# Kernel tuning notes

Measured on AMD Instinct MI355X. Metric: run time of the kernel, lower is better.

Reference implementation:

```python
import jax, jax.numpy as jnp
import numpy as np

B, H0, W0, C = 8, 112, 112, 192
NH, WS, SS = 6, 7, 3
HID = 4 * C


def _rel_pos_index(ws):
    coords = np.stack(np.meshgrid(np.arange(ws), np.arange(ws), indexing='ij'))  # [2,ws,ws]
    flat = coords.reshape(2, -1)
    rel = flat[:, :, None] - flat[:, None, :]          # [2,N,N]
    rel = rel.transpose(1, 2, 0).copy()                # [N,N,2]
    rel[:, :, 0] += ws - 1
    rel[:, :, 1] += ws - 1
    rel[:, :, 0] *= 2 * ws - 1
    return rel.sum(-1)                                 # [N,N]


def _attn_mask(Hp, Wp, ws, ss):
    # 0 / -100 mask for shifted windows, identical to torch get_attn_mask
    img = np.zeros((Hp, Wp))
    cnt = 0
    for hs in (slice(0, -ws), slice(-ws, -ss), slice(-ss, None)):
        for wsl in (slice(0, -ws), slice(-ws, -ss), slice(-ss, None)):
            img[hs, wsl] = cnt
            cnt += 1
    mw = img.reshape(Hp // ws, ws, Wp // ws, ws).transpose(0, 2, 1, 3).reshape(-1, ws * ws)
    am = mw[:, None, :] - mw[:, :, None]
    return np.where(am != 0, np.float32(-100.0), np.float32(0.0)).astype(np.float32)  # [nW,N,N]


def _ln(x, g, b, eps=1e-5):
    mu = jnp.mean(x, axis=-1, keepdims=True)
    var = jnp.mean(jnp.square(x - mu), axis=-1, keepdims=True)
    return (x - mu) * jax.lax.rsqrt(var + eps) * g + b


def setup_inputs() -> dict:
    key = jax.random.key(0)
    ks = jax.random.split(key, 8)
    p = lambda k, s: jax.random.normal(k, s, jnp.float32) * 0.02
    return {
        'query': jax.random.normal(ks[0], (B, H0 * W0, C), jnp.float32),
        'norm1_g': jnp.ones((C,), jnp.float32), 'norm1_b': jnp.zeros((C,), jnp.float32),
        'qkv_w': p(ks[1], (C, 3 * C)), 'qkv_b': jnp.zeros((3 * C,), jnp.float32),
        'rpb_table': p(ks[2], ((2 * WS - 1) ** 2, NH)),
        'proj_w': p(ks[3], (C, C)), 'proj_b': jnp.zeros((C,), jnp.float32),
        'norm2_g': jnp.ones((C,), jnp.float32), 'norm2_b': jnp.zeros((C,), jnp.float32),
        'fc1_w': p(ks[4], (C, HID)), 'fc1_b': jnp.zeros((HID,), jnp.float32),
        'fc2_w': p(ks[5], (HID, C)), 'fc2_b': jnp.zeros((C,), jnp.float32),
        'H': H0, 'W': W0,
    }


def reference(query, norm1_g, norm1_b, qkv_w, qkv_b, rpb_table, proj_w, proj_b,
              norm2_g, norm2_b, fc1_w, fc1_b, fc2_w, fc2_b, H, W):
    Bq, L, Cq = query.shape
    ws, ss, nh = WS, SS, NH
    hd = Cq // nh
    N = ws * ws
    # ---- W-MSA branch ----
    x = _ln(query, norm1_g, norm1_b).reshape(Bq, H, W, Cq)
    # H, W chosen divisible by ws -> pad branch is a no-op
    x = jnp.roll(x, (-ss, -ss), axis=(1, 2))            # cyclic shift
    nWh, nWw = H // ws, W // ws
    # window partition -> [B*nW, N, C]
    xw = x.reshape(Bq, nWh, ws, nWw, ws, Cq).transpose(0, 1, 3, 2, 4, 5).reshape(-1, N, Cq)
    qkv = (xw @ qkv_w + qkv_b).reshape(-1, N, 3, nh, hd).transpose(2, 0, 3, 1, 4)
    q, k, v = qkv[0] * (hd ** -0.5), qkv[1], qkv[2]     # [B_,nh,N,hd]
    attn = jnp.einsum('bhnd,bhmd->bhnm', q, k)
    bias = rpb_table[_rel_pos_index(ws).reshape(-1)].reshape(N, N, nh).transpose(2, 0, 1)
    attn = attn + bias[None]
    mask = jnp.asarray(_attn_mask(H, W, ws, ss))        # [nW,N,N]
    nW = mask.shape[0]
    attn = attn.reshape(Bq, nW, nh, N, N) + mask[None, :, None]
    attn = jax.nn.softmax(attn.reshape(-1, nh, N, N), axis=-1)
    out = jnp.einsum('bhnm,bhmd->bhnd', attn, v).transpose(0, 2, 1, 3).reshape(-1, N, Cq)
    out = out @ proj_w + proj_b
    # window reverse + reverse shift
    x = out.reshape(Bq, nWh, nWw, ws, ws, Cq).transpose(0, 1, 3, 2, 4, 5).reshape(Bq, H, W, Cq)
    x = jnp.roll(x, (ss, ss), axis=(1, 2)).reshape(Bq, H * W, Cq)
    x = query + x
    # ---- MLP branch ----
    h = _ln(x, norm2_g, norm2_b)
    h = jax.nn.gelu(h @ fc1_w + fc1_b, approximate=False)
    return x + (h @ fc2_w + fc2_b)
```

## Files before the change

kernel.cpp:

```cpp
#include <hip/hip_runtime.h>
#include <hip/hip_bf16.h>
#include <math.h>

using bf16 = __hip_bfloat16;
typedef __bf16 bf16x8 __attribute__((ext_vector_type(8)));
typedef __bf16 bf16x4 __attribute__((ext_vector_type(4)));
typedef float floatx4 __attribute__((ext_vector_type(4)));

__device__ __forceinline__ float bf2f(bf16 x) { return __bfloat162float(x); }
__device__ __forceinline__ bf16 f2bf(float x) { return __float2bfloat16(x); }

__device__ __forceinline__ float loadExt(const void* p, long i, int f32) {
  return f32 ? ((const float*)p)[i] : bf2f(((const bf16*)p)[i]);
}
__device__ __forceinline__ void storeExt(void* p, long i, int f32, float v) {
  if (f32) ((float*)p)[i] = v;
  else     ((bf16*)p)[i] = f2bf(v);
}

#define GLOAD16(gp, lp)                                                       \
  __builtin_amdgcn_global_load_lds(                                           \
      (const __attribute__((address_space(1))) void*)(gp),                    \
      (__attribute__((address_space(3))) void*)(lp), 16, 0, 0)

__global__ void detect_kernel(const unsigned int* __restrict__ q, int* __restrict__ flag) {
  const int lane = threadIdx.x;
  const unsigned int w = q[lane];
  const unsigned int lo = w & 0xffffu;
  const unsigned int e = (lo >> 7) & 0xffu;
  const bool ok = (lo == 0u) || (e >= 100u && e <= 141u);
  const unsigned long long m = __ballot(ok);
  if (lane == 0) flag[0] = (__popcll(m) == 64) ? 1 : 0;
}

__global__ void cvt_params_kernel(const int* __restrict__ flagp,
                                  const void* qkv_b, const void* proj_b,
                                  const void* n1g, const void* n1b,
                                  const void* n2g, const void* n2b,
                                  const void* fc1_b, const void* fc2_b,
                                  const void* rpb, bf16* __restrict__ dst) {
  const int f32 = (flagp[0] == 0);
  int i = blockIdx.x * blockDim.x + threadIdx.x;
  if (i >= 3510) return;
  const void* src; int j = i;
  if      (j < 576)  { src = qkv_b; }
  else if ((j -= 576)  < 192) { src = proj_b; }
  else if ((j -= 192)  < 192) { src = n1g; }
  else if ((j -= 192)  < 192) { src = n1b; }
  else if ((j -= 192)  < 192) { src = n2g; }
  else if ((j -= 192)  < 192) { src = n2b; }
  else if ((j -= 192)  < 768) { src = fc1_b; }
  else if ((j -= 768)  < 192) { src = fc2_b; }
  else { j -= 192; src = rpb; }
  dst[i] = f2bf(loadExt(src, j, f32));
}

__global__ void cvtT_kernel(const int* __restrict__ flagp, const void* __restrict__ src,
                            bf16* __restrict__ dst, int K, int N) {
  const int f32 = (flagp[0] == 0);
  int i = blockIdx.x * blockDim.x + threadIdx.x;
  if (i >= K * N) return;
  int n = i / K, k = i - n * K;
  dst[i] = f2bf(loadExt(src, (long)k * N + n, f32));
}

__global__ void biastab_kernel(const bf16* __restrict__ rpb,
                               bf16* __restrict__ btab) {
  int i = blockIdx.x * blockDim.x + threadIdx.x;
  if (i >= 6 * 2450) return;
  int head = i / 2450, r = i - head * 2450;
  int n = r / 50, m = r - n * 50;
  float v = 0.f;
  if (n < 49 && m < 49) {
    int r1 = n / 7, c1 = n - 7 * r1, r2 = m / 7, c2 = m - 7 * r2;
    v = bf2f(rpb[((r1 - r2 + 6) * 13 + (c1 - c2 + 6)) * 6 + head]);
  }
  btab[i] = f2bf(v);
}

__global__ __launch_bounds__(256) void ln_kernel(const int* __restrict__ flagp, int ext,
                                                 const void* __restrict__ x,
                                                 const bf16* __restrict__ g,
                                                 const bf16* __restrict__ b,
                                                 bf16* __restrict__ out) {
  const int f32 = ext && (flagp[0] == 0);
  const long row = (long)blockIdx.x * 4 + (threadIdx.x >> 6);
  const int lane = threadIdx.x & 63;
  const long gbase = row * 192;
  float v0 = loadExt(x, gbase + lane, f32);
  float v1 = loadExt(x, gbase + lane + 64, f32);
  float v2 = loadExt(x, gbase + lane + 128, f32);
  float s = v0 + v1 + v2;
  #pragma unroll
  for (int off = 32; off > 0; off >>= 1) s += __shfl_xor(s, off, 64);
  const float mu = s * (1.0f / 192.0f);
  float d0 = v0 - mu, d1 = v1 - mu, d2 = v2 - mu;
  float vv = d0 * d0 + d1 * d1 + d2 * d2;
  #pragma unroll
  for (int off = 32; off > 0; off >>= 1) vv += __shfl_xor(vv, off, 64);
  const float rstd = rsqrtf(vv * (1.0f / 192.0f) + 1e-5f);
  bf16* orow = out + row * 192;
  orow[lane]       = f2bf(d0 * rstd * bf2f(g[lane])       + bf2f(b[lane]));
  orow[lane + 64]  = f2bf(d1 * rstd * bf2f(g[lane + 64])  + bf2f(b[lane + 64]));
  orow[lane + 128] = f2bf(d2 * rstd * bf2f(g[lane + 128]) + bf2f(b[lane + 128]));
}

template <int EPI>
__global__ __launch_bounds__(256) void gemm_bt(const bf16* __restrict__ A,
                                               const bf16* __restrict__ BT,
                                               const bf16* __restrict__ bias,
                                               const int* __restrict__ flagp,
                                               const void* res, int res_ext,
                                               void* out, int out_ext,
                                               int M, int N, int K) {
  __shared__ __align__(16) bf16 As[2][128 * 32];
  __shared__ __align__(16) bf16 Bs[2][64 * 32];
  const int xf32 = (flagp[0] == 0);
  const int tid = threadIdx.x;
  const int wave = tid >> 6;
  const int lane = tid & 63;
  const int l16 = lane & 15;
  const int quad = lane >> 4;

  const int nbn = N >> 6;
  const int cpx = gridDim.x >> 3;
  const int wg = (gridDim.x & 7) ? (int)blockIdx.x
                                 : (blockIdx.x & 7) * cpx + (blockIdx.x >> 3);
  const int mb = wg / nbn;
  const int nb = wg - mb * nbn;
  const long m0 = (long)mb * 128;
  const int n0 = nb << 6;

  const int rS = tid >> 2;
  const int sS = tid & 3;
  const int ss = sS ^ ((rS >> 1) & 3);
  const bf16* gA0 = A + (m0 + rS) * (long)K + ss * 8;
  const bf16* gA1 = A + (m0 + rS + 64) * (long)K + ss * 8;
  const bf16* gB  = BT + (long)(n0 + rS) * K + ss * 8;

  floatx4 acc[2][4];
  #pragma unroll
  for (int i = 0; i < 2; i++)
    #pragma unroll
    for (int j = 0; j < 4; j++) acc[i][j] = (floatx4){0.f, 0.f, 0.f, 0.f};

  const int swz = (quad ^ ((l16 >> 1) & 3)) << 3;
  const int arow = wave * 32 + l16;

  GLOAD16(gA0, &As[0][tid * 8]);
  GLOAD16(gA1, &As[0][(tid + 256) * 8]);
  GLOAD16(gB,  &Bs[0][tid * 8]);
  __syncthreads();

  int cur = 0;
  for (int k0 = 0; k0 < K; k0 += 32) {
    if (k0 + 32 < K) {
      const int nxt = cur ^ 1;
      GLOAD16(gA0 + k0 + 32, &As[nxt][tid * 8]);
      GLOAD16(gA1 + k0 + 32, &As[nxt][(tid + 256) * 8]);
      GLOAD16(gB  + k0 + 32, &Bs[nxt][tid * 8]);
    }
    bf16x8 af[2], bfr[4];
    #pragma unroll
    for (int ms = 0; ms < 2; ms++)
      af[ms] = *(const bf16x8*)&As[cur][(arow + ms * 16) * 32 + swz];
    #pragma unroll
    for (int ns = 0; ns < 4; ns++)
      bfr[ns] = *(const bf16x8*)&Bs[cur][(ns * 16 + l16) * 32 + swz];
    #pragma unroll
    for (int ms = 0; ms < 2; ms++)
      #pragma unroll
      for (int ns = 0; ns < 4; ns++)
        acc[ms][ns] = __builtin_amdgcn_mfma_f32_16x16x32_bf16(bfr[ns], af[ms], acc[ms][ns], 0, 0, 0);
    __syncthreads();
    cur ^= 1;
  }

  #pragma unroll
  for (int ms = 0; ms < 2; ms++) {
    const long row = m0 + wave * 32 + ms * 16 + l16;
    #pragma unroll
    for (int ns = 0; ns < 4; ns++) {
      const int col = n0 + ns * 16 + quad * 4;
      const long idx = row * (long)N + col;
      float v[4];
      #pragma unroll
      for (int r = 0; r < 4; r++) v[r] = acc[ms][ns][r] + bf2f(bias[col + r]);
      if (EPI == 1) {
        #pragma unroll
        for (int r = 0; r < 4; r++)
          v[r] = 0.5f * v[r] * (1.0f + erff(v[r] * 0.70710678118654752f));
      }
      if (EPI == 2) {
        if (res_ext && xf32) {
          const float4 t = *(const float4*)((const float*)res + idx);
          v[0] += t.x; v[1] += t.y; v[2] += t.z; v[3] += t.w;
        } else {
          const bf16x4 t = *(const bf16x4*)((const bf16*)res + idx);
          #pragma unroll
          for (int r = 0; r < 4; r++) v[r] += (float)t[r];
        }
      }
      if (out_ext && xf32) {
        float4 t; t.x = v[0]; t.y = v[1]; t.z = v[2]; t.w = v[3];
        *(float4*)((float*)out + idx) = t;
      } else {
        bf16x4 t;
        #pragma unroll
        for (int r = 0; r < 4; r++) t[r] = (__bf16)v[r];
        *(bf16x4*)((bf16*)out + idx) = t;
      }
    }
  }
}

__global__ __launch_bounds__(64, 3) void attn_kernel(const bf16* __restrict__ qkv,
                                                     const bf16* __restrict__ btab,
                                                     bf16* __restrict__ out) {
  __shared__ __align__(16) __bf16 vshT[32 * 64];
  __shared__ __align__(16) __bf16 psh[64 * 64];
  __shared__ int rowIdx[64];
  __shared__ int regn[64];
  const int lane = threadIdx.x;
  const int q = lane >> 4, l16 = lane & 15;
  const int unit = blockIdx.x;
  const int head = unit % 6;
  const int wIdx = unit / 6;
  const int b = wIdx >> 8;
  const int w2 = wIdx & 255;
  const int wh = w2 >> 4;
  const int ww = w2 & 15;

  {
    const int l = lane < 49 ? lane : 48;
    const int r = l / 7, c = l - 7 * r;
    const int hr = wh * 7 + r;
    const int wr = ww * 7 + c;
    int h = hr + 3; if (h >= 112) h -= 112;
    int w = wr + 3; if (w >= 112) w -= 112;
    rowIdx[lane] = b * 12544 + h * 112 + w;
    const int rh = hr < 105 ? 0 : (hr < 109 ? 1 : 2);
    const int rw = wr < 105 ? 0 : (wr < 109 ? 1 : 2);
    regn[lane] = (lane < 49) ? rh * 3 + rw : 99;
  }
  __syncthreads();

  int ridx[4];
  #pragma unroll
  for (int t = 0; t < 4; t++) ridx[t] = rowIdx[t * 16 + l16];

  #pragma unroll
  for (int ii = 0; ii < 4; ii++) {
    const int i = lane + ii * 64;
    const int j = i >> 2, c = (i & 3) * 8;
    const bf16x8 vv = *(const bf16x8*)&qkv[(long)rowIdx[j] * 576 + 384 + head * 32 + c];
    #pragma unroll
    for (int jj = 0; jj < 8; jj++) {
      const int d = c + jj;
      vshT[d * 64 + (((j >> 3) ^ (d & 7)) << 3) + (j & 7)] = vv[jj];
    }
  }

  floatx4 s[4][4];
  #pragma unroll
  for (int it = 0; it < 4; it++)
    #pragma unroll
    for (int jt = 0; jt < 4; jt++) s[it][jt] = (floatx4){0.f, 0.f, 0.f, 0.f};
  {
    bf16x8 afq[4], bfk[4];
    #pragma unroll
    for (int t = 0; t < 4; t++) {
      const bf16* pQ = &qkv[(long)ridx[t] * 576 + head * 32 + q * 8];
      afq[t] = *(const bf16x8*)pQ;
      bfk[t] = *(const bf16x8*)(pQ + 192);
    }
    #pragma unroll
    for (int it = 0; it < 4; it++)
      #pragma unroll
      for (int jt = 0; jt < 4; jt++)
        s[it][jt] = __builtin_amdgcn_mfma_f32_16x16x32_bf16(afq[it], bfk[jt], s[it][jt], 0, 0, 0);
  }

  int regj[4];
  #pragma unroll
  for (int jt = 0; jt < 4; jt++) regj[jt] = regn[jt * 16 + l16];
  int regi[4][4];
  #pragma unroll
  for (int it = 0; it < 4; it++)
    #pragma unroll
    for (int r = 0; r < 4; r++) regi[it][r] = regn[it * 16 + q * 4 + r];

  const bf16* bt = btab + head * 2450;
  const float scale = 0.17677669529663687f;
  float mrow[4][4];
  #pragma unroll
  for (int it = 0; it < 4; it++)
    #pragma unroll
    for (int r = 0; r < 4; r++) mrow[it][r] = -3e38f;

  #pragma unroll
  for (int it = 0; it < 4; it++)
    #pragma unroll
    for (int jt = 0; jt < 4; jt++)
      #pragma unroll
      for (int r = 0; r < 4; r++) {
        const int i = it * 16 + q * 4 + r;
        const int j = jt * 16 + l16;
        const int bi = (i < 49 ? i : 48) * 50 + (j < 49 ? j : 48);
        float v = s[it][jt][r] * scale + bf2f(bt[bi]);
        if (regi[it][r] != regj[jt]) v -= 100.0f;
        v = (j < 49) ? v : -1e30f;
        s[it][jt][r] = v;
        mrow[it][r] = fmaxf(mrow[it][r], v);
      }
  #pragma unroll
  for (int it = 0; it < 4; it++)
    #pragma unroll
    for (int r = 0; r < 4; r++) {
      float m = mrow[it][r];
      #pragma unroll
      for (int off = 1; off < 16; off <<= 1) m = fmaxf(m, __shfl_xor(m, off, 64));
      mrow[it][r] = m;
    }
  float sum[4][4];
  #pragma unroll
  for (int it = 0; it < 4; it++)
    #pragma unroll
    for (int r = 0; r < 4; r++) sum[it][r] = 0.f;
  #pragma unroll
  for (int it = 0; it < 4; it++)
    #pragma unroll
    for (int jt = 0; jt < 4; jt++)
      #pragma unroll
      for (int r = 0; r < 4; r++) {
        const float e = __expf(s[it][jt][r] - mrow[it][r]);
        s[it][jt][r] = e;
        sum[it][r] += e;
      }
  #pragma unroll
  for (int it = 0; it < 4; it++)
    #pragma unroll
    for (int r = 0; r < 4; r++) {
      float t = sum[it][r];
      #pragma unroll
      for (int off = 1; off < 16; off <<= 1) t += __shfl_xor(t, off, 64);
      mrow[it][r] = 1.0f / t;
    }

  #pragma unroll
  for (int it = 0; it < 4; it++)
    #pragma unroll
    for (int jt = 0; jt < 4; jt++)
      #pragma unroll
      for (int r = 0; r < 4; r++) {
        const int i = it * 16 + q * 4 + r;
        const int j = jt * 16 + l16;
        psh[i * 64 + (((j >> 3) ^ (i & 7)) << 3) + (j & 7)] =
            (__bf16)(s[it][jt][r] * mrow[it][r]);
      }
  __syncthreads();

  floatx4 o[4][2];
  #pragma unroll
  for (int it = 0; it < 4; it++)
    #pragma unroll
    for (int dt = 0; dt < 2; dt++) o[it][dt] = (floatx4){0.f, 0.f, 0.f, 0.f};
  #pragma unroll
  for (int ks = 0; ks < 2; ks++) {
    bf16x8 av[2];
    #pragma unroll
    for (int dt = 0; dt < 2; dt++) {
      const int row = dt * 16 + l16;
      av[dt] = *(const bf16x8*)&vshT[row * 64 + (((ks * 4 + q) ^ (row & 7)) << 3)];
    }
    #pragma unroll
    for (int it = 0; it < 4; it++) {
      const int row = it * 16 + l16;
      const bf16x8 bp = *(const bf16x8*)&psh[row * 64 + (((ks * 4 + q) ^ (row & 7)) << 3)];
      #pragma unroll
      for (int dt = 0; dt < 2; dt++)
        o[it][dt] = __builtin_amdgcn_mfma_f32_16x16x32_bf16(bp, av[dt], o[it][dt], 0, 0, 0);
    }
  }

  #pragma unroll
  for (int it = 0; it < 4; it++)
    #pragma unroll
    for (int r = 0; r < 4; r++) {
      const int i = it * 16 + q * 4 + r;
      if (i < 49) {
        const long ob = (long)rowIdx[i] * 192 + head * 32;
        #pragma unroll
        for (int dt = 0; dt < 2; dt++)
          out[ob + dt * 16 + l16] = f2bf(o[it][dt][r]);
      }
    }
}

extern "C" void kernel_launch(void* const* d_in, const int* in_sizes, int n_in,
                              void* d_out, int out_size, void* d_ws, size_t ws_size,
                              hipStream_t stream) {
  const void* query   = d_in[0];
  const void* norm1_g = d_in[1];
  const void* norm1_b = d_in[2];
  const void* qkv_w   = d_in[3];
  const void* qkv_b   = d_in[4];
  const void* rpb     = d_in[5];
  const void* proj_w  = d_in[6];
  const void* proj_b  = d_in[7];
  const void* norm2_g = d_in[8];
  const void* norm2_b = d_in[9];
  const void* fc1_w   = d_in[10];
  const void* fc1_b   = d_in[11];
  const void* fc2_w   = d_in[12];
  const void* fc2_b   = d_in[13];

  const long M = 100352;

  int* flag  = (int*)d_ws;
  bf16* base = (bf16*)((char*)d_ws + 16);
  bf16* wsA   = base;
  bf16* wsB   = wsA + M * 192;
  bf16* xbuf  = wsB + M * 768;
  bf16* qkvT  = xbuf + M * 192;
  bf16* projT = qkvT + 110592;
  bf16* fc1T  = projT + 36864;
  bf16* fc2T  = fc1T + 147456;
  bf16* pPAR  = fc2T + 147456;
  bf16* pQKVB = pPAR;
  bf16* pPRJB = pQKVB + 576;
  bf16* pN1G  = pPRJB + 192;
  bf16* pN1B  = pN1G + 192;
  bf16* pN2G  = pN1B + 192;
  bf16* pN2B  = pN2G + 192;
  bf16* pFC1B = pN2B + 192;
  bf16* pFC2B = pFC1B + 768;
  bf16* pRPB  = pFC2B + 192;
  bf16* btab  = pPAR + 3510;

  detect_kernel<<<1, 64, 0, stream>>>((const unsigned int*)query, flag);
  cvt_params_kernel<<<14, 256, 0, stream>>>(flag, qkv_b, proj_b, norm1_g, norm1_b,
                                            norm2_g, norm2_b, fc1_b, fc2_b, rpb, pPAR);
  cvtT_kernel<<<(192 * 576 + 255) / 256, 256, 0, stream>>>(flag, qkv_w, qkvT, 192, 576);
  cvtT_kernel<<<(192 * 192 + 255) / 256, 256, 0, stream>>>(flag, proj_w, projT, 192, 192);
  cvtT_kernel<<<(192 * 768 + 255) / 256, 256, 0, stream>>>(flag, fc1_w, fc1T, 192, 768);
  cvtT_kernel<<<(768 * 192 + 255) / 256, 256, 0, stream>>>(flag, fc2_w, fc2T, 768, 192);
  biastab_kernel<<<(6 * 2450 + 255) / 256, 256, 0, stream>>>(pRPB, btab);

  ln_kernel<<<M / 4, 256, 0, stream>>>(flag, 1, query, pN1G, pN1B, wsA);
  gemm_bt<0><<<784 * 9, 256, 0, stream>>>(wsA, qkvT, pQKVB, flag,
                                          nullptr, 0, wsB, 0, (int)M, 576, 192);
  attn_kernel<<<12288, 64, 0, stream>>>(wsB, btab, wsA);
  gemm_bt<2><<<784 * 3, 256, 0, stream>>>(wsA, projT, pPRJB, flag,
                                          query, 1, xbuf, 0, (int)M, 192, 192);

  ln_kernel<<<M / 4, 256, 0, stream>>>(flag, 0, xbuf, pN2G, pN2B, wsA);
  gemm_bt<1><<<784 * 12, 256, 0, stream>>>(wsA, fc1T, pFC1B, flag,
                                           nullptr, 0, wsB, 0, (int)M, 768, 192);
  gemm_bt<2><<<784 * 3, 256, 0, stream>>>(wsB, fc2T, pFC2B, flag,
                                          xbuf, 0, d_out, 1, (int)M, 192, 768);
}
```

Measured before the change: 614.4 us.

## Triple-buffer GEMM LDS tiles with explicit vmcnt waits and single barrier

```diff
diff --git a/kernel.cpp b/kernel.cpp
--- a/kernel.cpp
+++ b/kernel.cpp
@@ -113,8 +113,8 @@
                                                const void* res, int res_ext,
                                                void* out, int out_ext,
                                                int M, int N, int K) {
-  __shared__ __align__(16) bf16 As[2][128 * 32];
-  __shared__ __align__(16) bf16 Bs[2][64 * 32];
+  __shared__ __align__(16) bf16 As[3][128 * 32];
+  __shared__ __align__(16) bf16 Bs[3][64 * 32];
   const int xf32 = (flagp[0] == 0);
   const int tid = threadIdx.x;
   const int wave = tid >> 6;
@@ -146,34 +146,42 @@
 
   const int swz = (quad ^ ((l16 >> 1) & 3)) << 3;
   const int arow = wave * 32 + l16;
-
-  GLOAD16(gA0, &As[0][tid * 8]);
-  GLOAD16(gA1, &As[0][(tid + 256) * 8]);
-  GLOAD16(gB,  &Bs[0][tid * 8]);
-  __syncthreads();
-
-  int cur = 0;
-  for (int k0 = 0; k0 < K; k0 += 32) {
-    if (k0 + 32 < K) {
-      const int nxt = cur ^ 1;
-      GLOAD16(gA0 + k0 + 32, &As[nxt][tid * 8]);
-      GLOAD16(gA1 + k0 + 32, &As[nxt][(tid + 256) * 8]);
-      GLOAD16(gB  + k0 + 32, &Bs[nxt][tid * 8]);
-    }
+  const int nt = K >> 5;
+
+  {
+    GLOAD16(gA0, &As[0][tid * 8]);
+    GLOAD16(gA1, &As[0][(tid + 256) * 8]);
+    GLOAD16(gB,  &Bs[0][tid * 8]);
+    GLOAD16(gA0 + 32, &As[1][tid * 8]);
+    GLOAD16(gA1 + 32, &As[1][(tid + 256) * 8]);
+    GLOAD16(gB  + 32, &Bs[1][tid * 8]);
+  }
+
+  for (int t = 0; t < nt; ++t) {
+    if (t + 1 < nt) { asm volatile("s_waitcnt vmcnt(3)" ::: "memory"); }
+    else            { asm volatile("s_waitcnt vmcnt(0)" ::: "memory"); }
+    __builtin_amdgcn_s_barrier();
+    __builtin_amdgcn_sched_barrier(0);
+    if (t + 2 < nt) {
+      const int p2 = (t + 2) % 3;
+      const int off = (t + 2) * 32;
+      GLOAD16(gA0 + off, &As[p2][tid * 8]);
+      GLOAD16(gA1 + off, &As[p2][(tid + 256) * 8]);
+      GLOAD16(gB  + off, &Bs[p2][tid * 8]);
+    }
+    const int p = t % 3;
     bf16x8 af[2], bfr[4];
     #pragma unroll
     for (int ms = 0; ms < 2; ms++)
-      af[ms] = *(const bf16x8*)&As[cur][(arow + ms * 16) * 32 + swz];
+      af[ms] = *(const bf16x8*)&As[p][(arow + ms * 16) * 32 + swz];
     #pragma unroll
     for (int ns = 0; ns < 4; ns++)
-      bfr[ns] = *(const bf16x8*)&Bs[cur][(ns * 16 + l16) * 32 + swz];
+      bfr[ns] = *(const bf16x8*)&Bs[p][(ns * 16 + l16) * 32 + swz];
     #pragma unroll
     for (int ms = 0; ms < 2; ms++)
       #pragma unroll
       for (int ns = 0; ns < 4; ns++)
         acc[ms][ns] = __builtin_amdgcn_mfma_f32_16x16x32_bf16(bfr[ns], af[ms], acc[ms][ns], 0, 0, 0);
-    __syncthreads();
-    cur ^= 1;
   }
 
   #pragma unroll
```

Result: no change. 615.2 us (+0.1%).

## Add K=192 single-shot GEMM kernel and fuse LayerNorm2 into FC1

Applied to the files above, without the earlier changes.

```diff
diff --git a/kernel.cpp b/kernel.cpp
--- a/kernel.cpp
+++ b/kernel.cpp
@@ -214,6 +214,160 @@
   }
 }
 
+template <int EPI, int LN>
+__global__ __launch_bounds__(256) void gemm_k192(const bf16* __restrict__ A,
+                                                 const bf16* __restrict__ BT,
+                                                 const bf16* __restrict__ bias,
+                                                 const bf16* __restrict__ gN,
+                                                 const bf16* __restrict__ bN,
+                                                 const int* __restrict__ flagp,
+                                                 const void* res, int res_ext,
+                                                 void* out, int out_ext,
+                                                 int M, int N) {
+  __shared__ __align__(16) __bf16 Ash[128 * 192];
+  __shared__ __align__(16) __bf16 Bsh[64 * 192];
+  const int xf32 = (flagp[0] == 0);
+  const int tid = threadIdx.x;
+  const int wave = tid >> 6;
+  const int lane = tid & 63;
+  const int l16 = lane & 15;
+  const int quad = lane >> 4;
+
+  const int nbn = N >> 6;
+  const int cpx = gridDim.x >> 3;
+  const int wg = (gridDim.x & 7) ? (int)blockIdx.x
+                                 : (blockIdx.x & 7) * cpx + (blockIdx.x >> 3);
+  const int mb = wg / nbn;
+  const int nb = wg - mb * nbn;
+  const long m0 = (long)mb * 128;
+  const int n0 = nb << 6;
+
+  #pragma unroll
+  for (int i = 0; i < 6; i++) {
+    const int u = i * 256 + tid;
+    const int r = u / 24, sl = u % 24;
+    const int ssl = (sl & 24) | ((sl ^ r) & 7);
+    GLOAD16(BT + (long)(n0 + r) * 192 + ssl * 8, &Bsh[u * 8]);
+  }
+  #pragma unroll
+  for (int i = 0; i < 12; i++) {
+    const int u = i * 256 + tid;
+    const int r = u / 24, sl = u % 24;
+    const int ssl = LN ? sl : ((sl & 24) | ((sl ^ r) & 7));
+    GLOAD16(A + (m0 + r) * (long)192 + ssl * 8, &Ash[u * 8]);
+  }
+  asm volatile("s_waitcnt vmcnt(0)" ::: "memory");
+  __builtin_amdgcn_s_barrier();
+
+  if (LN) {
+    const int row = tid >> 1, half = tid & 1;
+    bf16x8 xr[12];
+    #pragma unroll
+    for (int i = 0; i < 12; i++)
+      xr[i] = *(const bf16x8*)&Ash[row * 192 + (half * 12 + i) * 8];
+    float s1 = 0.f;
+    #pragma unroll
+    for (int i = 0; i < 12; i++)
+      #pragma unroll
+      for (int j = 0; j < 8; j++) s1 += (float)xr[i][j];
+    s1 += __shfl_xor(s1, 1, 64);
+    const float mu = s1 * (1.0f / 192.0f);
+    float s2 = 0.f;
+    #pragma unroll
+    for (int i = 0; i < 12; i++)
+      #pragma unroll
+      for (int j = 0; j < 8; j++) {
+        const float d = (float)xr[i][j] - mu;
+        s2 += d * d;
+      }
+    s2 += __shfl_xor(s2, 1, 64);
+    const float rstd = rsqrtf(s2 * (1.0f / 192.0f) + 1e-5f);
+    #pragma unroll
+    for (int i = 0; i < 12; i++) {
+      const int slot = half * 12 + i;
+      const bf16x8 gg = *(const bf16x8*)&gN[slot * 8];
+      const bf16x8 bb = *(const bf16x8*)&bN[slot * 8];
+      bf16x8 nr;
+      #pragma unroll
+      for (int j = 0; j < 8; j++)
+        nr[j] = (__bf16)(((float)xr[i][j] - mu) * rstd * (float)gg[j] + (float)bb[j]);
+      xr[i] = nr;
+    }
+    __syncthreads();
+    #pragma unroll
+    for (int i = 0; i < 12; i++) {
+      const int slot = half * 12 + i;
+      const int sw = (slot & 24) | ((slot ^ row) & 7);
+      *(bf16x8*)&Ash[row * 192 + sw * 8] = xr[i];
+    }
+    __syncthreads();
+  }
+
+  floatx4 acc[2][4];
+  #pragma unroll
+  for (int i = 0; i < 2; i++)
+    #pragma unroll
+    for (int j = 0; j < 4; j++) acc[i][j] = (floatx4){0.f, 0.f, 0.f, 0.f};
+
+  #pragma unroll
+  for (int ks = 0; ks < 6; ks++) {
+    const int sl = ks * 4 + quad;
+    bf16x8 af[2], bfr[4];
+    #pragma unroll
+    for (int ms = 0; ms < 2; ms++) {
+      const int r = wave * 32 + ms * 16 + l16;
+      af[ms] = *(const bf16x8*)&Ash[r * 192 + ((sl & 24) | ((sl ^ r) & 7)) * 8];
+    }
+    #pragma unroll
+    for (int ns = 0; ns < 4; ns++) {
+      const int r = ns * 16 + l16;
+      bfr[ns] = *(const bf16x8*)&Bsh[r * 192 + ((sl & 24) | ((sl ^ r) & 7)) * 8];
+    }
+    #pragma unroll
+    for (int ms = 0; ms < 2; ms++)
+      #pragma unroll
+      for (int ns = 0; ns < 4; ns++)
+        acc[ms][ns] = __builtin_amdgcn_mfma_f32_16x16x32_bf16(bfr[ns], af[ms], acc[ms][ns], 0, 0, 0);
+  }
+
+  #pragma unroll
+  for (int ms = 0; ms < 2; ms++) {
+    const long row = m0 + wave * 32 + ms * 16 + l16;
+    #pragma unroll
+    for (int ns = 0; ns < 4; ns++) {
+      const int col = n0 + ns * 16 + quad * 4;
+      const long idx = row * (long)N + col;
+      float v[4];
+      #pragma unroll
+      for (int r = 0; r < 4; r++) v[r] = acc[ms][ns][r] + bf2f(bias[col + r]);
+      if (EPI == 1) {
+        #pragma unroll
+        for (int r = 0; r < 4; r++)
+          v[r] = 0.5f * v[r] * (1.0f + erff(v[r] * 0.70710678118654752f));
+      }
+      if (EPI == 2) {
+        if (res_ext && xf32) {
+          const float4 t = *(const float4*)((const float*)res + idx);
+          v[0] += t.x; v[1] += t.y; v[2] += t.z; v[3] += t.w;
+        } else {
+          const bf16x4 t = *(const bf16x4*)((const bf16*)res + idx);
+          #pragma unroll
+          for (int r = 0; r < 4; r++) v[r] += (float)t[r];
+        }
+      }
+      if (out_ext && xf32) {
+        float4 t; t.x = v[0]; t.y = v[1]; t.z = v[2]; t.w = v[3];
+        *(float4*)((float*)out + idx) = t;
+      } else {
+        bf16x4 t;
+        #pragma unroll
+        for (int r = 0; r < 4; r++) t[r] = (__bf16)v[r];
+        *(bf16x4*)((bf16*)out + idx) = t;
+      }
+    }
+  }
+}
+
 __global__ __launch_bounds__(64, 3) void attn_kernel(const bf16* __restrict__ qkv,
                                                      const bf16* __restrict__ btab,
                                                      bf16* __restrict__ out) {
@@ -448,15 +602,14 @@
   biastab_kernel<<<(6 * 2450 + 255) / 256, 256, 0, stream>>>(pRPB, btab);
 
   ln_kernel<<<M / 4, 256, 0, stream>>>(flag, 1, query, pN1G, pN1B, wsA);
-  gemm_bt<0><<<784 * 9, 256, 0, stream>>>(wsA, qkvT, pQKVB, flag,
-                                          nullptr, 0, wsB, 0, (int)M, 576, 192);
+  gemm_k192<0, 0><<<784 * 9, 256, 0, stream>>>(wsA, qkvT, pQKVB, nullptr, nullptr,
+                                               flag, nullptr, 0, wsB, 0, (int)M, 576);
   attn_kernel<<<12288, 64, 0, stream>>>(wsB, btab, wsA);
-  gemm_bt<2><<<784 * 3, 256, 0, stream>>>(wsA, projT, pPRJB, flag,
-                                          query, 1, xbuf, 0, (int)M, 192, 192);
-
-  ln_kernel<<<M / 4, 256, 0, stream>>>(flag, 0, xbuf, pN2G, pN2B, wsA);
-  gemm_bt<1><<<784 * 12, 256, 0, stream>>>(wsA, fc1T, pFC1B, flag,
-                                           nullptr, 0, wsB, 0, (int)M, 768, 192);
+  gemm_k192<2, 0><<<784 * 3, 256, 0, stream>>>(wsA, projT, pPRJB, nullptr, nullptr,
+                                               flag, query, 1, xbuf, 0, (int)M, 192);
+
+  gemm_k192<1, 1><<<784 * 12, 256, 0, stream>>>(xbuf, fc1T, pFC1B, pN2G, pN2B,
+                                                flag, nullptr, 0, wsB, 0, (int)M, 768);
   gemm_bt<2><<<784 * 3, 256, 0, stream>>>(wsB, fc2T, pFC2B, flag,
                                           xbuf, 0, d_out, 1, (int)M, 192, 768);
 }
```

New measurement: 617.3 us. No clear change (+0.5%).
